# Optimization experiments

Measured on AMD Instinct MI355X. Metric: run time of the kernel, lower is better.

Reference implementation:

```python
import jax, jax.numpy as jnp
import numpy as np

B, T, V = 64, 2048, 512  # batch, max sequence length, vocab_size


def setup_inputs() -> dict:
    key = jax.random.key(0)
    k1, k2, k3, k4 = jax.random.split(key, 4)
    # times: increasing event times (unused by the model's math, but a forward arg)
    times = jnp.cumsum(jax.random.uniform(k1, (B, T), dtype=jnp.float32), axis=1)
    # codes: sparse binary multi-hot code occurrences per visit
    codes = (jax.random.uniform(k2, (B, T, V)) < 0.05).astype(jnp.float32)
    # lengths in [2, T]; force max length = T so padded output width T-1 matches
    # the original's max(lengths)-1
    lengths = jax.random.randint(k3, (B,), 2, T + 1, dtype=jnp.int32)
    lengths = lengths.at[0].set(T)
    # nn.Linear(V, V): xavier_uniform weight, zero bias
    limit = float(np.sqrt(6.0 / (V + V)))
    W = jax.random.uniform(k4, (V, V), minval=-limit, maxval=limit, dtype=jnp.float32)
    b = jnp.zeros((V,), dtype=jnp.float32)
    return {"times": times, "codes": codes, "lengths": lengths, "W": W, "b": b}


def reference(times, codes, lengths, W, b):
    # Prediction k (k = 1..seq_len-1) uses clamp(sum of first k code vectors, 0, 1),
    # i.e. cumsum index k-1. So valid prefix states are cumsum[:, :T-1].
    cum = jnp.clip(jnp.cumsum(codes, axis=1), 0.0, 1.0)[:, :-1]  # [B, T-1, V]
    # Single batched GEMM replacing B*T tiny per-vector Linear calls
    logits = jnp.einsum('btv,uv->btu', cum, W) + b  # [B, T-1, V]
    # Position j is valid iff j < lengths[b] - 1 (patients with len < 2 get all zeros)
    mask = jnp.arange(cum.shape[1])[None, :] < (lengths[:, None] - 1)  # [B, T-1]
    return jnp.where(mask[:, :, None], logits, 0.0)
```

## Files before the change

kernel.cpp:

```cpp
#include <hip/hip_runtime.h>
#include <stdint.h>

#define BB 64
#define TT 2048
#define VV 512
#define TOUT 2047
#define NCH 32
#define CH 64
#define NSUB 128
#define NEARLY 8
#define EV 8

typedef unsigned long long ull;
typedef float f32x4 __attribute__((ext_vector_type(4)));


__global__ void k_transpose(const float* __restrict__ W, float* __restrict__ wT) {
  __shared__ float tile[32][33];
  int bx = blockIdx.x, by = blockIdx.y;
  int tx = threadIdx.x, ty = threadIdx.y;
#pragma unroll
  for (int i = 0; i < 4; ++i)
    tile[ty + i * 8][tx] = W[(size_t)(by * 32 + ty + i * 8) * VV + bx * 32 + tx];
  __syncthreads();
#pragma unroll
  for (int i = 0; i < 4; ++i)
    wT[(size_t)(bx * 32 + ty + i * 8) * VV + by * 32 + tx] = tile[tx][ty + i * 8];
}

__global__ void k_rowsum(const float* __restrict__ W, const float* __restrict__ bias,
                         float* __restrict__ S) {
  int u = blockIdx.x;
  int l = threadIdx.x;
  const float* row = W + (size_t)u * VV;
  float4 a = *(const float4*)(row + 4 * l);
  float4 c = *(const float4*)(row + 256 + 4 * l);
  float s = a.x + a.y + a.z + a.w + c.x + c.y + c.z + c.w;
#pragma unroll
  for (int off = 32; off; off >>= 1) s += __shfl_xor(s, off, 64);
  if (l == 0) S[u] = bias[u] + s;
}

__global__ void k_maskpass(const float* __restrict__ codes, const int* __restrict__ lengths,
                           uint32_t* __restrict__ stash, uint32_t* __restrict__ submask) {
  int b = blockIdx.y;
  int sub = blockIdx.x;
  int tid = threadIdx.x, lane = tid & 63, w = tid >> 6;
  int validB = min(lengths[b] - 1, TOUT);
  int tstart = sub * 16 + w * 4;
  int n = min(4, validB - tstart);
  ull o0 = 0, o1 = 0, o2 = 0, o3 = 0, o4 = 0, o5 = 0, o6 = 0, o7 = 0;
  int ww = lane & 15, s = ww >> 1;
  int jmine = lane >> 4;
  uint32_t myval = 0;
  if (n > 0) {
    const float* cp0 = codes + ((size_t)b * TT + tstart) * VV;
    f32x4 fa[4], fb[4];
#pragma unroll
    for (int j = 0; j < 4; ++j)
      if (j < n) {
        const float* cp = cp0 + (size_t)j * VV;
        fa[j] = __builtin_nontemporal_load((const f32x4*)(cp + 4 * lane));
        fb[j] = __builtin_nontemporal_load((const f32x4*)(cp + 256 + 4 * lane));
      }
#pragma unroll
    for (int j = 0; j < 4; ++j)
      if (j < n) {
        ull b0 = __ballot(fa[j][0] != 0.f);
        ull b1 = __ballot(fa[j][1] != 0.f);
        ull b2 = __ballot(fa[j][2] != 0.f);
        ull b3 = __ballot(fa[j][3] != 0.f);
        ull b4 = __ballot(fb[j][0] != 0.f);
        ull b5 = __ballot(fb[j][1] != 0.f);
        ull b6 = __ballot(fb[j][2] != 0.f);
        ull b7 = __ballot(fb[j][3] != 0.f);
        o0 |= b0; o1 |= b1; o2 |= b2; o3 |= b3;
        o4 |= b4; o5 |= b5; o6 |= b6; o7 |= b7;
        ull m01 = (s & 1) ? b1 : b0;
        ull m23 = (s & 1) ? b3 : b2;
        ull m45 = (s & 1) ? b5 : b4;
        ull m67 = (s & 1) ? b7 : b6;
        ull m03 = (s & 2) ? m23 : m01;
        ull m47 = (s & 2) ? m67 : m45;
        ull mm = (s & 4) ? m47 : m03;
        uint32_t val = (ww & 1) ? (uint32_t)(mm >> 32) : (uint32_t)mm;
        if (j == jmine) myval = val;
      }
    if (jmine < n)
      stash[((size_t)b * TOUT + tstart) * 16 + lane] = myval;
  }
  __shared__ ull red[4][8];
  if (lane == 0) {
    red[w][0] = o0; red[w][1] = o1; red[w][2] = o2; red[w][3] = o3;
    red[w][4] = o4; red[w][5] = o5; red[w][6] = o6; red[w][7] = o7;
  }
  __syncthreads();
  if (tid < 16) {
    int sl = tid >> 1, h = tid & 1;
    ull m = red[0][sl] | red[1][sl] | red[2][sl] | red[3][sl];
    uint32_t v = h ? (uint32_t)(m >> 32) : (uint32_t)m;
    int wd = ((sl >> 2) << 3) | ((sl & 3) << 1) | h;
    submask[((size_t)b * NSUB + sub) * 16 + wd] = v;
  }
}

__device__ __forceinline__ int decode_v(int w, int k) {
  return ((w >> 3) << 8) | ((w & 1) << 7) | (k << 2) | ((w >> 1) & 3);
}
__device__ __forceinline__ int dec64(int s, int k) {
  return ((s >> 2) << 8) | (k << 2) | (s & 3);
}

__device__ __forceinline__ void add_bits4(uint32_t bits, int ww, int col,
                                          const float* __restrict__ wT,
                                          f32x4& L) {
#pragma unroll 1
  while (bits) {
    int k0 = __ffs(bits) - 1; bits &= bits - 1;
    int k1 = -1, k2 = -1, k3 = -1;
    if (bits) { k1 = __ffs(bits) - 1; bits &= bits - 1; }
    if (bits) { k2 = __ffs(bits) - 1; bits &= bits - 1; }
    if (bits) { k3 = __ffs(bits) - 1; bits &= bits - 1; }
    f32x4 f0 = *(const f32x4*)(wT + (size_t)decode_v(ww, k0) * VV + col);
    f32x4 acc = f0;
    if (k1 >= 0) { f32x4 f1 = *(const f32x4*)(wT + (size_t)decode_v(ww, k1) * VV + col);
                   acc += f1; }
    if (k2 >= 0) { f32x4 f2 = *(const f32x4*)(wT + (size_t)decode_v(ww, k2) * VV + col);
                   acc += f2; }
    if (k3 >= 0) { f32x4 f3 = *(const f32x4*)(wT + (size_t)decode_v(ww, k3) * VV + col);
                   acc += f3; }
    L += acc;
  }
}

__device__ __forceinline__ void build_bs(uint32_t wreg, ull* bs) {
#pragma unroll
  for (int s2 = 0; s2 < 8; ++s2) {
    uint32_t lo = (uint32_t)__shfl((int)wreg, 2 * s2, 64);
    uint32_t hi = (uint32_t)__shfl((int)wreg, 2 * s2 + 1, 64);
    bs[s2] = ((ull)hi << 32) | lo;
  }
}

__device__ __forceinline__ void accum_bitset(const ull* bs, int col,
                                             const float* __restrict__ wT,
                                             float sign, f32x4& L) {
  f32x4 a0 = {0.f, 0.f, 0.f, 0.f}, a1 = a0, a2 = a0, a3 = a0;
  int s = 0;
  ull cur = bs[0];
#define NEXT(vk)                                        \
  do {                                                  \
    while (cur == 0 && s < 7) { ++s; cur = bs[s]; }     \
    if (cur) { int kk = __ffsll(cur) - 1; cur &= cur - 1; vk = dec64(s, kk); } \
  } while (0)
  for (;;) {
    int v0 = -1, v1 = -1, v2 = -1, v3 = -1, v4 = -1, v5 = -1, v6 = -1, v7 = -1;
    NEXT(v0); NEXT(v1); NEXT(v2); NEXT(v3);
    NEXT(v4); NEXT(v5); NEXT(v6); NEXT(v7);
    if (v0 < 0) break;
    f32x4 f0, f1, f2, f3, f4, f5, f6, f7;
    f0 = *(const f32x4*)(wT + (size_t)v0 * VV + col);
    if (v1 >= 0) f1 = *(const f32x4*)(wT + (size_t)v1 * VV + col);
    if (v2 >= 0) f2 = *(const f32x4*)(wT + (size_t)v2 * VV + col);
    if (v3 >= 0) f3 = *(const f32x4*)(wT + (size_t)v3 * VV + col);
    if (v4 >= 0) f4 = *(const f32x4*)(wT + (size_t)v4 * VV + col);
    if (v5 >= 0) f5 = *(const f32x4*)(wT + (size_t)v5 * VV + col);
    if (v6 >= 0) f6 = *(const f32x4*)(wT + (size_t)v6 * VV + col);
    if (v7 >= 0) f7 = *(const f32x4*)(wT + (size_t)v7 * VV + col);
    a0 += f0;
    if (v1 >= 0) a1 += f1;
    if (v2 >= 0) a2 += f2;
    if (v3 >= 0) a3 += f3;
    if (v4 >= 0) a0 += f4;
    if (v5 >= 0) a1 += f5;
    if (v6 >= 0) a2 += f6;
    if (v7 >= 0) a3 += f7;
    if (v7 < 0) break;
  }
#undef NEXT
  f32x4 t = (a0 + a1) + (a2 + a3);
  L += sign * t;
}

__global__ void k_scan(const float* __restrict__ wT, const float* __restrict__ S,
                       const float* __restrict__ bias, const int* __restrict__ lengths,
                       float* __restrict__ outw, const uint32_t* __restrict__ stash,
                       const uint32_t* __restrict__ submask) {
  int b = blockIdx.y;
  int x = blockIdx.x;
  int tid = threadIdx.x, lane = tid & 63, w = tid >> 6;
  int col = w * 256 + 4 * lane;
  int myw = lane & 15;
  int validB = min(lengths[b] - 1, TOUT);
  bool early = (x < NEARLY);
  int t0, t1;
  if (early) { t0 = x * EV; t1 = t0 + EV; }
  else {
    int sw = (x - NEARLY) + (b % 31);
    if (sw >= 31) sw -= 31;
    t0 = (1 + sw) * CH; t1 = min(t0 + CH, TOUT);
  }
  int pe = min(t1, validB);

  if (t0 < pe) {
    uint32_t Pw = 0;
    if (early) {
      const uint32_t* st = stash + (size_t)b * TOUT * 16 + myw;
      uint32_t q0 = 0, q1 = 0, q2 = 0, q3 = 0, q4 = 0, q5 = 0, q6 = 0, q7 = 0;
      int t = 0;
      for (; t + 8 <= t0; t += 8) {
        q0 |= st[(t + 0) * 16]; q1 |= st[(t + 1) * 16];
        q2 |= st[(t + 2) * 16]; q3 |= st[(t + 3) * 16];
        q4 |= st[(t + 4) * 16]; q5 |= st[(t + 5) * 16];
        q6 |= st[(t + 6) * 16]; q7 |= st[(t + 7) * 16];
      }
      for (; t < t0; ++t) q0 |= st[t * 16];
      Pw = (q0 | q1) | (q2 | q3) | ((q4 | q5) | (q6 | q7));
    } else {
      const uint32_t* sm = submask + (size_t)b * NSUB * 16 + myw;
      int send = t0 >> 4;
      uint32_t p0 = 0, p1 = 0, p2 = 0, p3 = 0;
      int ss = 0;
      for (; ss + 4 <= send; ss += 4) {
        p0 |= sm[(ss + 0) * 16]; p1 |= sm[(ss + 1) * 16];
        p2 |= sm[(ss + 2) * 16]; p3 |= sm[(ss + 3) * 16];
      }
      for (; ss < send; ++ss) p0 |= sm[ss * 16];
      Pw = p0 | p1 | p2 | p3;
    }
    ull bs[8];
    build_bs(Pw, bs);
    int pc = 0;
#pragma unroll
    for (int s2 = 0; s2 < 8; ++s2) pc += __popcll(bs[s2]);
    bool direct = (pc <= 256);
    f32x4 L;
    if (direct) {
      L = *(const f32x4*)(bias + col);
      accum_bitset(bs, col, wT, 1.f, L);
    } else {
      L = *(const f32x4*)(S + col);
      ull nb[8];
#pragma unroll
      for (int s2 = 0; s2 < 8; ++s2) nb[s2] = ~bs[s2];
      accum_bitset(nb, col, wT, -1.f, L);
    }

    float* ob = outw + (size_t)b * TOUT * VV + col;
    const uint32_t* st = stash + (size_t)b * TOUT * 16 + myw;
    if (early) {
      int n = pe - t0;
      uint32_t vm[EV];
#pragma unroll
      for (int i = 0; i < EV; ++i)
        if (i < n) vm[i] = st[(size_t)(t0 + i) * 16];
#pragma unroll 1
      for (int i = 0; i < n; ++i) {
        uint32_t cand = vm[i] & ~Pw;
        uint32_t wwm = (uint32_t)__ballot(cand != 0) & 0xFFFFu;
        Pw |= cand;
        while (wwm) {
          int ww = __ffs(wwm) - 1; wwm &= wwm - 1;
          uint32_t nbw = (uint32_t)__shfl((int)cand, ww, 64);
          add_bits4(nbw, ww, col, wT, L);
        }
        __builtin_nontemporal_store(L, (f32x4*)(ob + (size_t)(t0 + i) * VV));
      }
    } else {
      int nfull = (pe - t0) >> 4;
      uint32_t vmr[16], vmn[16];
      if (nfull > 0) {
#pragma unroll
        for (int i = 0; i < 16; ++i) vmr[i] = st[(size_t)(t0 + i) * 16];
      }
#pragma unroll 1
      for (int ib = 0; ib < nfull; ++ib) {
        int base = t0 + ib * 16;
        if (ib + 1 < nfull) {
#pragma unroll
          for (int i = 0; i < 16; ++i) vmn[i] = st[(size_t)(base + 16 + i) * 16];
        }
#pragma unroll
        for (int i = 0; i < 16; ++i) {
          uint32_t cand = vmr[i] & ~Pw;
          uint32_t wwm = (uint32_t)__ballot(cand != 0) & 0xFFFFu;
          Pw |= cand;
          while (wwm) {
            int ww = __ffs(wwm) - 1; wwm &= wwm - 1;
            uint32_t nbw = (uint32_t)__shfl((int)cand, ww, 64);
            add_bits4(nbw, ww, col, wT, L);
          }
          __builtin_nontemporal_store(L, (f32x4*)(ob + (size_t)(base + i) * VV));
        }
#pragma unroll
        for (int i = 0; i < 16; ++i) vmr[i] = vmn[i];
      }
#pragma unroll 1
      for (int t = t0 + nfull * 16; t < pe; ++t) {
        uint32_t cand = st[(size_t)t * 16] & ~Pw;
        uint32_t wwm = (uint32_t)__ballot(cand != 0) & 0xFFFFu;
        Pw |= cand;
        while (wwm) {
          int ww = __ffs(wwm) - 1; wwm &= wwm - 1;
          uint32_t nbw = (uint32_t)__shfl((int)cand, ww, 64);
          add_bits4(nbw, ww, col, wT, L);
        }
        __builtin_nontemporal_store(L, (f32x4*)(ob + (size_t)t * VV));
      }
    }
  }
  int z0 = max(t0, validB);
  if (z0 < t1) {
    size_t basep = (size_t)(b * TOUT + z0) * VV;
    size_t n = (size_t)(t1 - z0) * VV;
    f32x4 z = {0.f, 0.f, 0.f, 0.f};
    for (size_t i = (size_t)tid * 4; i < n; i += 128 * 4)
      __builtin_nontemporal_store(z, (f32x4*)(outw + basep + i));
  }
}

extern "C" void kernel_launch(void* const* d_in, const int* in_sizes, int n_in,
                              void* d_out, int out_size, void* d_ws, size_t ws_size,
                              hipStream_t stream) {
  const float* codes = (const float*)d_in[1];
  const int* lengths = (const int*)d_in[2];
  const float* W = (const float*)d_in[3];
  const float* bias = (const float*)d_in[4];
  float* out = (float*)d_out;

  char* ws = (char*)d_ws;
  float* wT = (float*)ws;
  float* S = (float*)(ws + 0x100000);
  uint32_t* submask = (uint32_t*)(ws + 0x110000);
  uint32_t* stash = (uint32_t*)(ws + 0x200000);

  k_maskpass<<<dim3(NSUB, BB), dim3(256), 0, stream>>>(codes, lengths, stash, submask);
  k_transpose<<<dim3(16, 16), dim3(32, 8), 0, stream>>>(W, wT);
  k_rowsum<<<dim3(512), dim3(64), 0, stream>>>(W, bias, S);
  k_scan<<<dim3(NEARLY + 31, BB), dim3(128), 0, stream>>>(wT, S, bias, lengths,
                                                          out, stash, submask);
}
```

Measured before the change: 459.6 us.

## Precompute per-chunk prefix logits and masks in a serial init kernel

Adds a k_init kernel that walks each batch row once, incrementally accumulating W columns for newly set codes, and stores the starting logits vector and presence mask for every early group and every chunk. k_scan then loads these starting states instead of rebuilding the prefix mask and summing up to 256 W rows per block, and the rowsum/complement trick is dropped. This removes redundant per-block prefix work, but adds a serial per-batch pass (64 blocks of 128 threads) plus an extra launch and workspace traffic on the critical path.

```diff
diff --git a/kernel.cpp b/kernel.cpp
--- a/kernel.cpp
+++ b/kernel.cpp
@@ -26,19 +26,6 @@
 #pragma unroll
   for (int i = 0; i < 4; ++i)
     wT[(size_t)(bx * 32 + ty + i * 8) * VV + by * 32 + tx] = tile[tx][ty + i * 8];
-}
-
-__global__ void k_rowsum(const float* __restrict__ W, const float* __restrict__ bias,
-                         float* __restrict__ S) {
-  int u = blockIdx.x;
-  int l = threadIdx.x;
-  const float* row = W + (size_t)u * VV;
-  float4 a = *(const float4*)(row + 4 * l);
-  float4 c = *(const float4*)(row + 256 + 4 * l);
-  float s = a.x + a.y + a.z + a.w + c.x + c.y + c.z + c.w;
-#pragma unroll
-  for (int off = 32; off; off >>= 1) s += __shfl_xor(s, off, 64);
-  if (l == 0) S[u] = bias[u] + s;
 }
 
 __global__ void k_maskpass(const float* __restrict__ codes, const int* __restrict__ lengths,
@@ -144,7 +131,7 @@
 
 __device__ __forceinline__ void accum_bitset(const ull* bs, int col,
                                              const float* __restrict__ wT,
-                                             float sign, f32x4& L) {
+                                             f32x4& L) {
   f32x4 a0 = {0.f, 0.f, 0.f, 0.f}, a1 = a0, a2 = a0, a3 = a0;
   int s = 0;
   ull cur = bs[0];
@@ -178,14 +165,65 @@
     if (v7 < 0) break;
   }
 #undef NEXT
-  f32x4 t = (a0 + a1) + (a2 + a3);
-  L += sign * t;
-}
-
-__global__ void k_scan(const float* __restrict__ wT, const float* __restrict__ S,
-                       const float* __restrict__ bias, const int* __restrict__ lengths,
+  L += (a0 + a1) + (a2 + a3);
+}
+
+__global__ void k_init(const float* __restrict__ wT, const float* __restrict__ bias,
+                       const int* __restrict__ lengths,
+                       const uint32_t* __restrict__ stash,
+                       const uint32_t* __restrict__ submask,
+                       float* __restrict__ L0e, float* __restrict__ L0c,
+                       uint32_t* __restrict__ Pe, uint32_t* __restrict__ Pc) {
+  int b = blockIdx.x;
+  int tid = threadIdx.x, lane = tid & 63, w = tid >> 6;
+  int col = w * 256 + 4 * lane;
+  int myw = lane & 15;
+  int validB = min(lengths[b] - 1, TOUT);
+  f32x4 L = *(const f32x4*)(bias + col);
+  uint32_t Pw = 0;
+  const uint32_t* st = stash + (size_t)b * TOUT * 16 + myw;
+#pragma unroll 1
+  for (int g = 0; g < NEARLY; ++g) {
+    *(f32x4*)(L0e + ((size_t)b * NEARLY + g) * VV + col) = L;
+    if (w == 0 && lane < 16) Pe[((size_t)b * NEARLY + g) * 16 + myw] = Pw;
+    int tb = g * EV;
+    int ne = min(EV, validB - tb);
+    if (ne > 0) {
+      uint32_t vv[EV];
+#pragma unroll
+      for (int i = 0; i < EV; ++i) vv[i] = (i < ne) ? st[(size_t)(tb + i) * 16] : 0u;
+      uint32_t om = (vv[0] | vv[1]) | (vv[2] | vv[3]) |
+                    ((vv[4] | vv[5]) | (vv[6] | vv[7]));
+      uint32_t cand = om & ~Pw;
+      if (__ballot(cand != 0)) {
+        ull cs[8]; build_bs(cand, cs);
+        accum_bitset(cs, col, wT, L);
+        Pw |= cand;
+      }
+    }
+  }
+  const uint32_t* sm = submask + (size_t)b * NSUB * 16 + myw;
+#pragma unroll 1
+  for (int c = 1; c < NCH; ++c) {
+    *(f32x4*)(L0c + ((size_t)b * NCH + c) * VV + col) = L;
+    if (w == 0 && lane < 16) Pc[((size_t)b * NCH + c) * 16 + myw] = Pw;
+    if (c == NCH - 1) break;
+    int s0 = c * 4;
+    uint32_t om = sm[(s0 + 0) * 16] | sm[(s0 + 1) * 16] |
+                  sm[(s0 + 2) * 16] | sm[(s0 + 3) * 16];
+    uint32_t cand = om & ~Pw;
+    if (__ballot(cand != 0)) {
+      ull cs[8]; build_bs(cand, cs);
+      accum_bitset(cs, col, wT, L);
+      Pw |= cand;
+    }
+  }
+}
+
+__global__ void k_scan(const float* __restrict__ wT, const int* __restrict__ lengths,
                        float* __restrict__ outw, const uint32_t* __restrict__ stash,
-                       const uint32_t* __restrict__ submask) {
+                       const float* __restrict__ L0e, const float* __restrict__ L0c,
+                       const uint32_t* __restrict__ Pe, const uint32_t* __restrict__ Pc) {
   int b = blockIdx.y;
   int x = blockIdx.x;
   int tid = threadIdx.x, lane = tid & 63, w = tid >> 6;
@@ -203,47 +241,15 @@
   int pe = min(t1, validB);
 
   if (t0 < pe) {
-    uint32_t Pw = 0;
+    uint32_t Pw;
+    f32x4 L;
     if (early) {
-      const uint32_t* st = stash + (size_t)b * TOUT * 16 + myw;
-      uint32_t q0 = 0, q1 = 0, q2 = 0, q3 = 0, q4 = 0, q5 = 0, q6 = 0, q7 = 0;
-      int t = 0;
-      for (; t + 8 <= t0; t += 8) {
-        q0 |= st[(t + 0) * 16]; q1 |= st[(t + 1) * 16];
-        q2 |= st[(t + 2) * 16]; q3 |= st[(t + 3) * 16];
-        q4 |= st[(t + 4) * 16]; q5 |= st[(t + 5) * 16];
-        q6 |= st[(t + 6) * 16]; q7 |= st[(t + 7) * 16];
-      }
-      for (; t < t0; ++t) q0 |= st[t * 16];
-      Pw = (q0 | q1) | (q2 | q3) | ((q4 | q5) | (q6 | q7));
+      Pw = Pe[((size_t)b * NEARLY + x) * 16 + myw];
+      L = *(const f32x4*)(L0e + ((size_t)b * NEARLY + x) * VV + col);
     } else {
-      const uint32_t* sm = submask + (size_t)b * NSUB * 16 + myw;
-      int send = t0 >> 4;
-      uint32_t p0 = 0, p1 = 0, p2 = 0, p3 = 0;
-      int ss = 0;
-      for (; ss + 4 <= send; ss += 4) {
-        p0 |= sm[(ss + 0) * 16]; p1 |= sm[(ss + 1) * 16];
-        p2 |= sm[(ss + 2) * 16]; p3 |= sm[(ss + 3) * 16];
-      }
-      for (; ss < send; ++ss) p0 |= sm[ss * 16];
-      Pw = p0 | p1 | p2 | p3;
-    }
-    ull bs[8];
-    build_bs(Pw, bs);
-    int pc = 0;
-#pragma unroll
-    for (int s2 = 0; s2 < 8; ++s2) pc += __popcll(bs[s2]);
-    bool direct = (pc <= 256);
-    f32x4 L;
-    if (direct) {
-      L = *(const f32x4*)(bias + col);
-      accum_bitset(bs, col, wT, 1.f, L);
-    } else {
-      L = *(const f32x4*)(S + col);
-      ull nb[8];
-#pragma unroll
-      for (int s2 = 0; s2 < 8; ++s2) nb[s2] = ~bs[s2];
-      accum_bitset(nb, col, wT, -1.f, L);
+      int c = t0 / CH;
+      Pw = Pc[((size_t)b * NCH + c) * 16 + myw];
+      L = *(const f32x4*)(L0c + ((size_t)b * NCH + c) * VV + col);
     }
 
     float* ob = outw + (size_t)b * TOUT * VV + col;
@@ -330,13 +336,17 @@
 
   char* ws = (char*)d_ws;
   float* wT = (float*)ws;
-  float* S = (float*)(ws + 0x100000);
-  uint32_t* submask = (uint32_t*)(ws + 0x110000);
-  uint32_t* stash = (uint32_t*)(ws + 0x200000);
+  float* L0e = (float*)(ws + 0x100000);
+  float* L0c = (float*)(ws + 0x200000);
+  uint32_t* Pe = (uint32_t*)(ws + 0x600000);
+  uint32_t* Pc = (uint32_t*)(ws + 0x610000);
+  uint32_t* submask = (uint32_t*)(ws + 0x640000);
+  uint32_t* stash = (uint32_t*)(ws + 0x700000);
 
   k_maskpass<<<dim3(NSUB, BB), dim3(256), 0, stream>>>(codes, lengths, stash, submask);
   k_transpose<<<dim3(16, 16), dim3(32, 8), 0, stream>>>(W, wT);
-  k_rowsum<<<dim3(512), dim3(64), 0, stream>>>(W, bias, S);
-  k_scan<<<dim3(NEARLY + 31, BB), dim3(128), 0, stream>>>(wT, S, bias, lengths,
-                                                          out, stash, submask);
-}
+  k_init<<<dim3(BB), dim3(128), 0, stream>>>(wT, bias, lengths, stash, submask,
+                                             L0e, L0c, Pe, Pc);
+  k_scan<<<dim3(NEARLY + 31, BB), dim3(128), 0, stream>>>(wT, lengths, out, stash,
+                                                          L0e, L0c, Pe, Pc);
+}
```

Result: slower. 528.2 us (+14.9%).
